# Performance work log

Hardware: AMD Instinct MI355X
Metric: run time of the kernel (lower is better)

The kernel has to match this reference:

```python
import jax, jax.numpy as jnp
import numpy as np

H = 64          # hidden_size
IN = 6          # input_size
PREDICT = 10    # predict_size


def _lstm_cell(x_t, h, c, Wih, Whh, bih, bhh):
    # PyTorch gate order: i, f, g, o ; gates = x W_ih^T + b_ih + h W_hh^T + b_hh
    g = x_t @ Wih.T + bih + h @ Whh.T + bhh            # [B, 4H]
    i, f, gg, o = jnp.split(g, 4, axis=-1)
    c_new = jax.nn.sigmoid(f) * c + jax.nn.sigmoid(i) * jnp.tanh(gg)
    h_new = jax.nn.sigmoid(o) * jnp.tanh(c_new)
    return h_new, c_new


def setup_inputs() -> dict:
    key = jax.random.key(0)
    ks = jax.random.split(key, 12)
    B, T = 4096, 1024
    s = 1.0 / np.sqrt(H)  # torch default uniform init bound
    u = lambda k, shape: jax.random.uniform(k, shape, jnp.float32, -s, s)
    return {
        "x": jax.random.normal(ks[0], (B, T, IN), jnp.float32),
        "W_ih0": u(ks[1], (4 * H, IN)),
        "W_hh0": u(ks[2], (4 * H, H)),
        "b_ih0": u(ks[3], (4 * H,)),
        "b_hh0": u(ks[4], (4 * H,)),
        "W_ih1": u(ks[5], (4 * H, H)),
        "W_hh1": u(ks[6], (4 * H, H)),
        "b_ih1": u(ks[7], (4 * H,)),
        "b_hh1": u(ks[8], (4 * H,)),
        "fc_w": u(ks[9], (IN, H)),
        "fc_b": u(ks[10], (IN,)),
    }


def reference(x, W_ih0, W_hh0, b_ih0, b_hh0, W_ih1, W_hh1, b_ih1, b_hh1, fc_w, fc_b):
    B = x.shape[0]
    zeros = jnp.zeros((B, H), x.dtype)
    init = (zeros, zeros, zeros, zeros)  # h0, c0, h1, c1

    def stacked_step(carry, x_t):
        h0, c0, h1, c1 = carry
        h0, c0 = _lstm_cell(x_t, h0, c0, W_ih0, W_hh0, b_ih0, b_hh0)
        h1, c1 = _lstm_cell(h0, h1, c1, W_ih1, W_hh1, b_ih1, b_hh1)
        return (h0, c0, h1, c1), None

    # Encoder: scan over time (batch_first -> transpose to [T, B, IN])
    carry, _ = jax.lax.scan(stacked_step, init, jnp.swapaxes(x, 0, 1))

    def dec_step(state, _):
        dec_in, c = state
        c, _ = stacked_step(c, dec_in)
        pred = c[0 + 2] @ fc_w.T + fc_b  # top-layer h -> [B, IN]
        return (pred, c), pred

    dec_in0 = x[:, -1, :]
    _, preds = jax.lax.scan(dec_step, (dec_in0, carry), None, length=PREDICT)
    return jnp.swapaxes(preds, 0, 1)  # [B, PREDICT, IN]
```

## Files before the change

### kernel.cpp

```cpp
#include <hip/hip_runtime.h>

#define T_SEQ   1024
#define INDIM   6
#define HDIM    64
#define NPRED   10
#define CHNK    128
#define S0      104
#define NROWS   16

typedef __bf16         bf16x8 __attribute__((ext_vector_type(8)));
typedef float          f32x4  __attribute__((ext_vector_type(4)));
typedef float          f32x2  __attribute__((ext_vector_type(2)));
typedef unsigned short us4    __attribute__((ext_vector_type(4)));

#define MFMA16(a, b, c) __builtin_amdgcn_mfma_f32_16x16x32_bf16((a), (b), (c), 0, 0, 0)

static __device__ __forceinline__ float bf2f(unsigned short b) {
  union { unsigned int u; float f; } v; v.u = ((unsigned int)b) << 16; return v.f;
}
static __device__ __forceinline__ unsigned short f2bf(float f) {
  union { __bf16 b; unsigned short u; } v; v.b = (__bf16)f; return v.u;
}

template <bool F32>
__global__ __launch_bounds__(512, 2)
void lstm2_pipe(const void* __restrict__ xv,
                const void* __restrict__ Wih0v,
                const void* __restrict__ Whh0v,
                const void* __restrict__ bih0v,
                const void* __restrict__ bhh0v,
                const void* __restrict__ Wih1v,
                const void* __restrict__ Whh1v,
                const void* __restrict__ bih1v,
                const void* __restrict__ bhh1v,
                const void* __restrict__ fcwv,
                const void* __restrict__ fcbv,
                void* __restrict__ outv)
{
  {
    const unsigned short* w0u = (const unsigned short*)Wih0v;
    int votes = 0;
#pragma unroll
    for (int i = 0; i < 16; ++i) {
      const unsigned e = (w0u[2 * i] >> 7) & 0xFF;
      votes += (e >= 0x80 || e <= 0x40) ? 1 : 0;
    }
    if ((votes >= 4) != F32) return;
  }

  __shared__ __align__(16) unsigned short A0[2][NROWS * S0];
  __shared__ __align__(16) unsigned short A1[2][NROWS * S0];
  __shared__ __align__(16) unsigned short XB[NROWS * CHNK * INDIM];
  __shared__ __align__(16) unsigned short FCW[INDIM * HDIM];
  __shared__ float FCB[INDIM];

  const int tid   = threadIdx.x;
  const int lane  = tid & 63;
  const int wave  = tid >> 6;
  const bool isA  = (wave < 4);
  const int  wv4  = wave & 3;
  const int  q    = lane >> 4;
  const int  n    = lane & 15;
  const int  u    = 16 * wv4 + n;
  const int rbase = blockIdx.x * NROWS;

  {
    unsigned short* p0 = &A0[0][0];
    unsigned short* p1 = &A1[0][0];
    for (int i = tid; i < 2 * NROWS * S0; i += 512) { p0[i] = 0; p1[i] = 0; }
  }
  for (int i = tid; i < INDIM * HDIM; i += 512) {
    if constexpr (F32) FCW[i] = f2bf(((const float*)fcwv)[i]);
    else               FCW[i] = ((const unsigned short*)fcwv)[i];
  }
  if (tid < INDIM) {
    if constexpr (F32) FCB[tid] = ((const float*)fcbv)[tid];
    else               FCB[tid] = bf2f(((const unsigned short*)fcbv)[tid]);
  }

  auto ld1 = [&](const void* p, int i) -> float {
    if constexpr (F32) return ((const float*)p)[i];
    else               return bf2f(((const unsigned short*)p)[i]);
  };
  auto ld8 = [&](const void* W, int off) -> bf16x8 {
    union { unsigned short us[8]; bf16x8 v; } t;
    if constexpr (F32) {
      const float* p = (const float*)W + off;
#pragma unroll
      for (int j = 0; j < 8; ++j) t.us[j] = f2bf(p[j]);
    } else {
      t.v = *(const bf16x8*)((const unsigned short*)W + off);
    }
    return t.v;
  };

  auto load_chunk = [&](int t0c) {
    if constexpr (F32) {
      const char* xb = (const char*)xv;
      for (int c = tid; c < NROWS * 192; c += 512) {
        const int row = c / 192;
        const int off = c - row * 192;
        const float4 v = *(const float4*)(xb + (size_t)(rbase + row) * (T_SEQ * INDIM * 4)
                                             + (size_t)t0c * (INDIM * 4) + (size_t)off * 16);
        us4 o;
        o.x = f2bf(v.x); o.y = f2bf(v.y); o.z = f2bf(v.z); o.w = f2bf(v.w);
        *(us4*)((char*)XB + (size_t)c * 8) = o;
      }
    } else {
      const char* xb = (const char*)xv;
      for (int c = tid; c < NROWS * 96; c += 512) {
        const int row = c / 96;
        const int off = c - row * 96;
        const int4 v = *(const int4*)(xb + (size_t)(rbase + row) * (T_SEQ * INDIM * 2)
                                         + (size_t)t0c * (INDIM * 2) + (size_t)off * 16);
        *(int4*)((char*)XB + (size_t)c * 16) = v;
      }
    }
  };

  load_chunk(0);
  __syncthreads();

  const int xrow   = tid / INDIM;
  const int xk     = tid - xrow * INDIM;
  const int xWrOff = xrow * S0 + HDIM + xk;
  const int xbBase = xrow * (CHNK * INDIM) + xk;

  if (tid < 96) A0[0][xWrOff] = XB[xbBase];
  __syncthreads();

  const int aOff  = n * S0 + 8 * q;
  const int hOffW = n * S0 + 16 * wv4 + 4 * q;
  const int bOff  = 16 * wv4 + 4 * q;

  f32x2 cc2[2]; cc2[0] = (f32x2){0.f, 0.f}; cc2[1] = (f32x2){0.f, 0.f};

  auto ldbias = [&](const void* b1, const void* b2, int gt) -> f32x4 {
    f32x4 r;
#pragma unroll
    for (int j = 0; j < 4; ++j)
      r[j] = ld1(b1, 64 * gt + bOff + j) + ld1(b2, 64 * gt + bOff + j);
    return r;
  };

  const f32x2 C1   = {-1.442695040888963f, -1.442695040888963f};
  const f32x2 C2   = {-2.885390081777927f, -2.885390081777927f};
  const f32x2 onep = {1.0f, 1.0f};

  auto act4 = [&](const f32x4 gI, const f32x4 gF, const f32x4 gG, const f32x4 gO,
                  unsigned short* dst) {
    unsigned int w2[2];
#pragma unroll
    for (int p = 0; p < 2; ++p) {
      f32x2 vI, vF, vG, vO;
      vI.x = gI[2 * p]; vI.y = gI[2 * p + 1];
      vF.x = gF[2 * p]; vF.y = gF[2 * p + 1];
      vG.x = gG[2 * p]; vG.y = gG[2 * p + 1];
      vO.x = gO[2 * p]; vO.y = gO[2 * p + 1];
      const f32x2 aF = vF * C1;
      const f32x2 aI = vI * C1;
      const f32x2 aG = vG * C2;
      const f32x2 aO = vO * C1;
      f32x2 Ae, Be, Ge, Oe;
      Ae.x = __builtin_amdgcn_exp2f(aF.x); Ae.y = __builtin_amdgcn_exp2f(aF.y);
      Be.x = __builtin_amdgcn_exp2f(aI.x); Be.y = __builtin_amdgcn_exp2f(aI.y);
      Ge.x = __builtin_amdgcn_exp2f(aG.x); Ge.y = __builtin_amdgcn_exp2f(aG.y);
      Oe.x = __builtin_amdgcn_exp2f(aO.x); Oe.y = __builtin_amdgcn_exp2f(aO.y);
      const f32x2 M1 = (onep + Be) * (onep + Ge);
      const f32x2 t2 = onep + Ae;
      const f32x2 nm = cc2[p] * M1 + (onep - Ge) * t2;
      const f32x2 den = t2 * M1;
      f32x2 rd; rd.x = __builtin_amdgcn_rcpf(den.x); rd.y = __builtin_amdgcn_rcpf(den.y);
      const f32x2 cn = nm * rd;
      cc2[p] = cn;
      const f32x2 aE = cn * C2;
      f32x2 Ee; Ee.x = __builtin_amdgcn_exp2f(aE.x); Ee.y = __builtin_amdgcn_exp2f(aE.y);
      const f32x2 dh = (onep + Ee) * (onep + Oe);
      f32x2 rh; rh.x = __builtin_amdgcn_rcpf(dh.x); rh.y = __builtin_amdgcn_rcpf(dh.y);
      const f32x2 hv = (onep - Ee) * rh;
      w2[p] = (unsigned int)f2bf(hv.x) | ((unsigned int)f2bf(hv.y) << 16);
    }
    uint2 pk; pk.x = w2[0]; pk.y = w2[1];
    *(uint2*)(dst + hOffW) = pk;
  };

  unsigned short* H0 = &A0[0][0];
  unsigned short* H1 = &A1[1][0];

  if (isA) {
    bf16x8 WA[12]; f32x4 bvA[4];
#pragma unroll
    for (int gt = 0; gt < 4; ++gt) {
      const int col = 64 * gt + u;
      WA[gt * 3 + 0] = ld8(Whh0v, col * HDIM + 8 * q);
      WA[gt * 3 + 1] = ld8(Whh0v, col * HDIM + 32 + 8 * q);
      union { unsigned short us[8]; bf16x8 v; } t2;
#pragma unroll
      for (int j = 0; j < 8; ++j) t2.us[j] = 0;
      if (q == 0) {
#pragma unroll
        for (int j = 0; j < INDIM; ++j) t2.us[j] = f2bf(ld1(Wih0v, col * INDIM + j));
      }
      WA[gt * 3 + 2] = t2.v;
      bvA[gt] = ldbias(bih0v, bhh0v, gt);
    }

    int t0v = 0;
    for (int i = 0; i <= T_SEQ; ++i) {
      if (((i + 1) & (CHNK - 1)) == 0 && (i + 1) < T_SEQ) {
        load_chunk(i + 1);
        __syncthreads();
        t0v = i + 1;
      }
      const int cur = i & 1;
      if (i < T_SEQ) {
        const unsigned short* A0c = &A0[cur][0];
        unsigned short*       A0n = &A0[cur ^ 1][0];
        const int srct = (i + 1 < T_SEQ) ? (i + 1) : (T_SEQ - 1);
        if (tid < 96) A0n[xWrOff] = XB[xbBase + (srct - t0v) * INDIM];
        const bf16x8 f0 = *(const bf16x8*)(A0c + aOff);
        const bf16x8 f1 = *(const bf16x8*)(A0c + aOff + 32);
        const bf16x8 f2 = *(const bf16x8*)(A0c + aOff + 64);
        f32x4 g0 = MFMA16(WA[0], f0, bvA[0]); g0 = MFMA16(WA[1],  f1, g0); g0 = MFMA16(WA[2],  f2, g0);
        f32x4 g1 = MFMA16(WA[3], f0, bvA[1]); g1 = MFMA16(WA[4],  f1, g1); g1 = MFMA16(WA[5],  f2, g1);
        f32x4 g2 = MFMA16(WA[6], f0, bvA[2]); g2 = MFMA16(WA[7],  f1, g2); g2 = MFMA16(WA[8],  f2, g2);
        f32x4 g3 = MFMA16(WA[9], f0, bvA[3]); g3 = MFMA16(WA[10], f1, g3); g3 = MFMA16(WA[11], f2, g3);
        act4(g0, g1, g2, g3, A0n);
      }
      __syncthreads();
    }
    for (int d = 0; d < NPRED; ++d) {
      const bf16x8 fa0 = *(const bf16x8*)(H0 + aOff);
      const bf16x8 fa1 = *(const bf16x8*)(H0 + aOff + 32);
      const bf16x8 fa2 = *(const bf16x8*)(H0 + aOff + 64);
      __syncthreads();
      {
        f32x4 g0 = MFMA16(WA[0], fa0, bvA[0]); g0 = MFMA16(WA[1],  fa1, g0); g0 = MFMA16(WA[2],  fa2, g0);
        f32x4 g1 = MFMA16(WA[3], fa0, bvA[1]); g1 = MFMA16(WA[4],  fa1, g1); g1 = MFMA16(WA[5],  fa2, g1);
        f32x4 g2 = MFMA16(WA[6], fa0, bvA[2]); g2 = MFMA16(WA[7],  fa1, g2); g2 = MFMA16(WA[8],  fa2, g2);
        f32x4 g3 = MFMA16(WA[9], fa0, bvA[3]); g3 = MFMA16(WA[10], fa1, g3); g3 = MFMA16(WA[11], fa2, g3);
        act4(g0, g1, g2, g3, H0);
      }
      __syncthreads();
      __syncthreads();
      if (tid < 96) {
        const unsigned short* h1row = H1 + xrow * S0;
        const int4* hp = (const int4*)h1row;
        const int4* wp = (const int4*)(&FCW[xk * HDIM]);
        float s = FCB[xk];
#pragma unroll
        for (int i8 = 0; i8 < 8; ++i8) {
          const int4 hv = hp[i8];
          const int4 wv2 = wp[i8];
          const unsigned int hu[4] = {(unsigned)hv.x, (unsigned)hv.y, (unsigned)hv.z, (unsigned)hv.w};
          const unsigned int wu[4] = {(unsigned)wv2.x, (unsigned)wv2.y, (unsigned)wv2.z, (unsigned)wv2.w};
#pragma unroll
          for (int k2 = 0; k2 < 4; ++k2) {
            union { unsigned int uu; float ff; } hl, hh2, wl, wh;
            hl.uu = hu[k2] << 16; hh2.uu = hu[k2] & 0xFFFF0000u;
            wl.uu = wu[k2] << 16; wh.uu  = wu[k2] & 0xFFFF0000u;
            s += hl.ff * wl.ff + hh2.ff * wh.ff;
          }
        }
        const unsigned short pb = f2bf(s);
        const size_t idx = (size_t)(rbase + xrow) * (NPRED * INDIM) + (size_t)d * INDIM + xk;
        if constexpr (F32) ((float*)outv)[idx] = s;
        else               ((unsigned short*)outv)[idx] = pb;
        H0[xWrOff] = pb;
      }
      __syncthreads();
    }
  } else {
    bf16x8 WB[16]; f32x4 bvB[4];
#pragma unroll
    for (int gt = 0; gt < 4; ++gt) {
      const int col = 64 * gt + u;
      WB[gt * 4 + 0] = ld8(Wih1v, col * HDIM + 8 * q);
      WB[gt * 4 + 1] = ld8(Wih1v, col * HDIM + 32 + 8 * q);
      WB[gt * 4 + 2] = ld8(Whh1v, col * HDIM + 8 * q);
      WB[gt * 4 + 3] = ld8(Whh1v, col * HDIM + 32 + 8 * q);
      bvB[gt] = ldbias(bih1v, bhh1v, gt);
    }

    for (int i = 0; i <= T_SEQ; ++i) {
      if (((i + 1) & (CHNK - 1)) == 0 && (i + 1) < T_SEQ) {
        load_chunk(i + 1);
        __syncthreads();
      }
      const int cur = i & 1;
      if (i >= 1) {
        const unsigned short* A0c = &A0[cur][0];
        const unsigned short* A1c = &A1[cur][0];
        unsigned short*       A1n = &A1[cur ^ 1][0];
        const bf16x8 h0a = *(const bf16x8*)(A0c + aOff);
        const bf16x8 h0b = *(const bf16x8*)(A0c + aOff + 32);
        const bf16x8 r0  = *(const bf16x8*)(A1c + aOff);
        const bf16x8 r1  = *(const bf16x8*)(A1c + aOff + 32);
        f32x4 g0 = MFMA16(WB[0],  h0a, bvB[0]); g0 = MFMA16(WB[1],  h0b, g0); g0 = MFMA16(WB[2],  r0, g0); g0 = MFMA16(WB[3],  r1, g0);
        f32x4 g1 = MFMA16(WB[4],  h0a, bvB[1]); g1 = MFMA16(WB[5],  h0b, g1); g1 = MFMA16(WB[6],  r0, g1); g1 = MFMA16(WB[7],  r1, g1);
        f32x4 g2 = MFMA16(WB[8],  h0a, bvB[2]); g2 = MFMA16(WB[9],  h0b, g2); g2 = MFMA16(WB[10], r0, g2); g2 = MFMA16(WB[11], r1, g2);
        f32x4 g3 = MFMA16(WB[12], h0a, bvB[3]); g3 = MFMA16(WB[13], h0b, g3); g3 = MFMA16(WB[14], r0, g3); g3 = MFMA16(WB[15], r1, g3);
        act4(g0, g1, g2, g3, A1n);
      }
      __syncthreads();
    }
    for (int d = 0; d < NPRED; ++d) {
      const bf16x8 fr0 = *(const bf16x8*)(H1 + aOff);
      const bf16x8 fr1 = *(const bf16x8*)(H1 + aOff + 32);
      __syncthreads();
      __syncthreads();
      {
        const bf16x8 h0a = *(const bf16x8*)(H0 + aOff);
        const bf16x8 h0b = *(const bf16x8*)(H0 + aOff + 32);
        f32x4 g0 = MFMA16(WB[0],  h0a, bvB[0]); g0 = MFMA16(WB[1],  h0b, g0); g0 = MFMA16(WB[2],  fr0, g0); g0 = MFMA16(WB[3],  fr1, g0);
        f32x4 g1 = MFMA16(WB[4],  h0a, bvB[1]); g1 = MFMA16(WB[5],  h0b, g1); g1 = MFMA16(WB[6],  fr0, g1); g1 = MFMA16(WB[7],  fr1, g1);
        f32x4 g2 = MFMA16(WB[8],  h0a, bvB[2]); g2 = MFMA16(WB[9],  h0b, g2); g2 = MFMA16(WB[10], fr0, g2); g2 = MFMA16(WB[11], fr1, g2);
        f32x4 g3 = MFMA16(WB[12], h0a, bvB[3]); g3 = MFMA16(WB[13], h0b, g3); g3 = MFMA16(WB[14], fr0, g3); g3 = MFMA16(WB[15], fr1, g3);
        act4(g0, g1, g2, g3, H1);
      }
      __syncthreads();
      __syncthreads();
    }
  }
}

extern "C" void kernel_launch(void* const* d_in, const int* in_sizes, int n_in,
                              void* d_out, int out_size, void* d_ws, size_t ws_size,
                              hipStream_t stream) {
  (void)in_sizes; (void)n_in; (void)d_ws; (void)ws_size; (void)out_size;
  const void* x    = d_in[0];
  const void* Wih0 = d_in[1];
  const void* Whh0 = d_in[2];
  const void* bih0 = d_in[3];
  const void* bhh0 = d_in[4];
  const void* Wih1 = d_in[5];
  const void* Whh1 = d_in[6];
  const void* bih1 = d_in[7];
  const void* bhh1 = d_in[8];
  const void* fcw  = d_in[9];
  const void* fcb  = d_in[10];
  lstm2_pipe<true><<<dim3(4096 / NROWS), dim3(512), 0, stream>>>(
      x, Wih0, Whh0, bih0, bhh0, Wih1, Whh1, bih1, bhh1, fcw, fcb, d_out);
  lstm2_pipe<false><<<dim3(4096 / NROWS), dim3(512), 0, stream>>>(
      x, Wih0, Whh0, bih0, bhh0, Wih1, Whh1, bih1, bhh1, fcw, fcb, d_out);
}
```

Before: 910.6 us.

## Split LSTM step into MFMA and activation phases to overlap layers

```diff
diff --git a/kernel.cpp b/kernel.cpp
--- a/kernel.cpp
+++ b/kernel.cpp
@@ -185,7 +185,7 @@
   };
 
   unsigned short* H0 = &A0[0][0];
-  unsigned short* H1 = &A1[1][0];
+  unsigned short* H1 = &A1[0][0];
 
   if (isA) {
     bf16x8 WA[12]; f32x4 bvA[4];
@@ -206,26 +206,31 @@
     }
 
     int t0v = 0;
-    for (int i = 0; i <= T_SEQ; ++i) {
+    f32x4 gA0, gA1, gA2, gA3;
+    for (int i = 0; i <= T_SEQ + 1; ++i) {
       if (((i + 1) & (CHNK - 1)) == 0 && (i + 1) < T_SEQ) {
         load_chunk(i + 1);
         __syncthreads();
         t0v = i + 1;
       }
       const int cur = i & 1;
-      if (i < T_SEQ) {
+      const bool run = (i < T_SEQ);
+      if (run) {
         const unsigned short* A0c = &A0[cur][0];
-        unsigned short*       A0n = &A0[cur ^ 1][0];
-        const int srct = (i + 1 < T_SEQ) ? (i + 1) : (T_SEQ - 1);
-        if (tid < 96) A0n[xWrOff] = XB[xbBase + (srct - t0v) * INDIM];
         const bf16x8 f0 = *(const bf16x8*)(A0c + aOff);
         const bf16x8 f1 = *(const bf16x8*)(A0c + aOff + 32);
         const bf16x8 f2 = *(const bf16x8*)(A0c + aOff + 64);
-        f32x4 g0 = MFMA16(WA[0], f0, bvA[0]); g0 = MFMA16(WA[1],  f1, g0); g0 = MFMA16(WA[2],  f2, g0);
-        f32x4 g1 = MFMA16(WA[3], f0, bvA[1]); g1 = MFMA16(WA[4],  f1, g1); g1 = MFMA16(WA[5],  f2, g1);
-        f32x4 g2 = MFMA16(WA[6], f0, bvA[2]); g2 = MFMA16(WA[7],  f1, g2); g2 = MFMA16(WA[8],  f2, g2);
-        f32x4 g3 = MFMA16(WA[9], f0, bvA[3]); g3 = MFMA16(WA[10], f1, g3); g3 = MFMA16(WA[11], f2, g3);
-        act4(g0, g1, g2, g3, A0n);
+        gA0 = MFMA16(WA[0], f0, bvA[0]); gA0 = MFMA16(WA[1],  f1, gA0); gA0 = MFMA16(WA[2],  f2, gA0);
+        gA1 = MFMA16(WA[3], f0, bvA[1]); gA1 = MFMA16(WA[4],  f1, gA1); gA1 = MFMA16(WA[5],  f2, gA1);
+        gA2 = MFMA16(WA[6], f0, bvA[2]); gA2 = MFMA16(WA[7],  f1, gA2); gA2 = MFMA16(WA[8],  f2, gA2);
+        gA3 = MFMA16(WA[9], f0, bvA[3]); gA3 = MFMA16(WA[10], f1, gA3); gA3 = MFMA16(WA[11], f2, gA3);
+      }
+      __syncthreads();
+      if (run) {
+        unsigned short* A0n = &A0[cur ^ 1][0];
+        const int srct = (i + 1 < T_SEQ) ? (i + 1) : (T_SEQ - 1);
+        if (tid < 96) A0n[xWrOff] = XB[xbBase + (srct - t0v) * INDIM];
+        act4(gA0, gA1, gA2, gA3, A0n);
       }
       __syncthreads();
     }
@@ -282,25 +287,28 @@
       bvB[gt] = ldbias(bih1v, bhh1v, gt);
     }
 
-    for (int i = 0; i <= T_SEQ; ++i) {
+    f32x4 gB0, gB1, gB2, gB3;
+    for (int i = 0; i <= T_SEQ + 1; ++i) {
       if (((i + 1) & (CHNK - 1)) == 0 && (i + 1) < T_SEQ) {
         load_chunk(i + 1);
         __syncthreads();
       }
       const int cur = i & 1;
-      if (i >= 1) {
+      if (i >= 2) {
+        act4(gB0, gB1, gB2, gB3, &A1[cur ^ 1][0]);
+      }
+      __syncthreads();
+      if (i >= 1 && i <= T_SEQ) {
         const unsigned short* A0c = &A0[cur][0];
-        const unsigned short* A1c = &A1[cur][0];
-        unsigned short*       A1n = &A1[cur ^ 1][0];
+        const unsigned short* A1c = &A1[cur ^ 1][0];
         const bf16x8 h0a = *(const bf16x8*)(A0c + aOff);
         const bf16x8 h0b = *(const bf16x8*)(A0c + aOff + 32);
         const bf16x8 r0  = *(const bf16x8*)(A1c + aOff);
         const bf16x8 r1  = *(const bf16x8*)(A1c + aOff + 32);
-        f32x4 g0 = MFMA16(WB[0],  h0a, bvB[0]); g0 = MFMA16(WB[1],  h0b, g0); g0 = MFMA16(WB[2],  r0, g0); g0 = MFMA16(WB[3],  r1, g0);
-        f32x4 g1 = MFMA16(WB[4],  h0a, bvB[1]); g1 = MFMA16(WB[5],  h0b, g1); g1 = MFMA16(WB[6],  r0, g1); g1 = MFMA16(WB[7],  r1, g1);
-        f32x4 g2 = MFMA16(WB[8],  h0a, bvB[2]); g2 = MFMA16(WB[9],  h0b, g2); g2 = MFMA16(WB[10], r0, g2); g2 = MFMA16(WB[11], r1, g2);
-        f32x4 g3 = MFMA16(WB[12], h0a, bvB[3]); g3 = MFMA16(WB[13], h0b, g3); g3 = MFMA16(WB[14], r0, g3); g3 = MFMA16(WB[15], r1, g3);
-        act4(g0, g1, g2, g3, A1n);
+        gB0 = MFMA16(WB[0],  h0a, bvB[0]); gB0 = MFMA16(WB[1],  h0b, gB0); gB0 = MFMA16(WB[2],  r0, gB0); gB0 = MFMA16(WB[3],  r1, gB0);
+        gB1 = MFMA16(WB[4],  h0a, bvB[1]); gB1 = MFMA16(WB[5],  h0b, gB1); gB1 = MFMA16(WB[6],  r0, gB1); gB1 = MFMA16(WB[7],  r1, gB1);
+        gB2 = MFMA16(WB[8],  h0a, bvB[2]); gB2 = MFMA16(WB[9],  h0b, gB2); gB2 = MFMA16(WB[10], r0, gB2); gB2 = MFMA16(WB[11], r1, gB2);
+        gB3 = MFMA16(WB[12], h0a, bvB[3]); gB3 = MFMA16(WB[13], h0b, gB3); gB3 = MFMA16(WB[14], r0, gB3); gB3 = MFMA16(WB[15], r1, gB3);
       }
       __syncthreads();
     }
```

Result: slower. 1.010 ms (+10.9%).

## Replace per-step block barriers with LDS flag polling between layer wave groups

Applied to the files above, without the earlier changes.

```diff
diff --git a/kernel.cpp b/kernel.cpp
--- a/kernel.cpp
+++ b/kernel.cpp
@@ -21,6 +21,7 @@
 static __device__ __forceinline__ unsigned short f2bf(float f) {
   union { __bf16 b; unsigned short u; } v; v.b = (__bf16)f; return v.u;
 }
+static __device__ __forceinline__ int imin(int a, int b) { return a < b ? a : b; }
 
 template <bool F32>
 __global__ __launch_bounds__(512, 2)
@@ -48,11 +49,12 @@
     if ((votes >= 4) != F32) return;
   }
 
-  __shared__ __align__(16) unsigned short A0[2][NROWS * S0];
+  __shared__ __align__(16) unsigned short A0[4][NROWS * S0];
   __shared__ __align__(16) unsigned short A1[2][NROWS * S0];
   __shared__ __align__(16) unsigned short XB[NROWS * CHNK * INDIM];
   __shared__ __align__(16) unsigned short FCW[INDIM * HDIM];
   __shared__ float FCB[INDIM];
+  __shared__ int FLG[8];
 
   const int tid   = threadIdx.x;
   const int lane  = tid & 63;
@@ -67,7 +69,8 @@
   {
     unsigned short* p0 = &A0[0][0];
     unsigned short* p1 = &A1[0][0];
-    for (int i = tid; i < 2 * NROWS * S0; i += 512) { p0[i] = 0; p1[i] = 0; }
+    for (int i = tid; i < 4 * NROWS * S0; i += 512) p0[i] = 0;
+    for (int i = tid; i < 2 * NROWS * S0; i += 512) p1[i] = 0;
   }
   for (int i = tid; i < INDIM * HDIM; i += 512) {
     if constexpr (F32) FCW[i] = f2bf(((const float*)fcwv)[i]);
@@ -77,6 +80,7 @@
     if constexpr (F32) FCB[tid] = ((const float*)fcbv)[tid];
     else               FCB[tid] = bf2f(((const unsigned short*)fcbv)[tid]);
   }
+  if (tid < 8) FLG[tid] = 0;
 
   auto ld1 = [&](const void* p, int i) -> float {
     if constexpr (F32) return ((const float*)p)[i];
@@ -121,17 +125,40 @@
   load_chunk(0);
   __syncthreads();
 
-  const int xrow   = tid / INDIM;
-  const int xk     = tid - xrow * INDIM;
-  const int xWrOff = xrow * S0 + HDIM + xk;
-  const int xbBase = xrow * (CHNK * INDIM) + xk;
-
-  if (tid < 96) A0[0][xWrOff] = XB[xbBase];
+  const int dxr    = tid / INDIM;
+  const int dxk    = tid - dxr * INDIM;
+  const int dxWrOff= dxr * S0 + HDIM + dxk;
+
+  if (tid < 96) A0[3][dxWrOff] = XB[dxr * (CHNK * INDIM) + dxk];
   __syncthreads();
+
+  const int  xe     = wv4 * 24 + lane;
+  const bool xact   = isA && (lane < 24);
+  const int  exr    = xe / INDIM;
+  const int  exk    = xe - exr * INDIM;
+  const int  exWrOff= exr * S0 + HDIM + exk;
+  const int  exbBase= exr * (CHNK * INDIM) + exk;
 
   const int aOff  = n * S0 + 8 * q;
   const int hOffW = n * S0 + 16 * wv4 + 4 * q;
   const int bOff  = 16 * wv4 + 4 * q;
+
+  auto poll2 = [&](int ta, int tb) {
+    volatile int* f = (volatile int*)FLG;
+    for (;;) {
+      const int a0 = f[0], a1 = f[1], a2 = f[2], a3 = f[3];
+      const int b0 = f[4], b1 = f[5], b2 = f[6], b3 = f[7];
+      const int am = imin(imin(a0, a1), imin(a2, a3));
+      const int bm = imin(imin(b0, b1), imin(b2, b3));
+      if (am >= ta && bm >= tb) break;
+      __builtin_amdgcn_s_sleep(1);
+    }
+    __threadfence_block();
+  };
+  auto post = [&](int idx, int val) {
+    __threadfence_block();
+    if (lane == 0) ((volatile int*)FLG)[idx] = val;
+  };
 
   f32x2 cc2[2]; cc2[0] = (f32x2){0.f, 0.f}; cc2[1] = (f32x2){0.f, 0.f};
 
@@ -184,7 +211,7 @@
     *(uint2*)(dst + hOffW) = pk;
   };
 
-  unsigned short* H0 = &A0[0][0];
+  unsigned short* H0 = &A0[3][0];
   unsigned short* H1 = &A1[1][0];
 
   if (isA) {
@@ -206,29 +233,29 @@
     }
 
     int t0v = 0;
-    for (int i = 0; i <= T_SEQ; ++i) {
-      if (((i + 1) & (CHNK - 1)) == 0 && (i + 1) < T_SEQ) {
-        load_chunk(i + 1);
+    for (int t = 0; t < T_SEQ; ++t) {
+      if (((t + 1) & (CHNK - 1)) == 0 && (t + 1) < T_SEQ) {
         __syncthreads();
-        t0v = i + 1;
-      }
-      const int cur = i & 1;
-      if (i < T_SEQ) {
-        const unsigned short* A0c = &A0[cur][0];
-        unsigned short*       A0n = &A0[cur ^ 1][0];
-        const int srct = (i + 1 < T_SEQ) ? (i + 1) : (T_SEQ - 1);
-        if (tid < 96) A0n[xWrOff] = XB[xbBase + (srct - t0v) * INDIM];
-        const bf16x8 f0 = *(const bf16x8*)(A0c + aOff);
-        const bf16x8 f1 = *(const bf16x8*)(A0c + aOff + 32);
-        const bf16x8 f2 = *(const bf16x8*)(A0c + aOff + 64);
-        f32x4 g0 = MFMA16(WA[0], f0, bvA[0]); g0 = MFMA16(WA[1],  f1, g0); g0 = MFMA16(WA[2],  f2, g0);
-        f32x4 g1 = MFMA16(WA[3], f0, bvA[1]); g1 = MFMA16(WA[4],  f1, g1); g1 = MFMA16(WA[5],  f2, g1);
-        f32x4 g2 = MFMA16(WA[6], f0, bvA[2]); g2 = MFMA16(WA[7],  f1, g2); g2 = MFMA16(WA[8],  f2, g2);
-        f32x4 g3 = MFMA16(WA[9], f0, bvA[3]); g3 = MFMA16(WA[10], f1, g3); g3 = MFMA16(WA[11], f2, g3);
-        act4(g0, g1, g2, g3, A0n);
-      }
-      __syncthreads();
-    }
+        load_chunk(t + 1);
+        __syncthreads();
+        t0v = t + 1;
+      }
+      poll2(t, t - 3);
+      const unsigned short* A0c = &A0[(t + 3) & 3][0];
+      unsigned short*       A0n = &A0[t & 3][0];
+      const int srct = (t + 1 < T_SEQ) ? (t + 1) : (T_SEQ - 1);
+      if (xact) A0n[exWrOff] = XB[exbBase + (srct - t0v) * INDIM];
+      const bf16x8 f0 = *(const bf16x8*)(A0c + aOff);
+      const bf16x8 f1 = *(const bf16x8*)(A0c + aOff + 32);
+      const bf16x8 f2 = *(const bf16x8*)(A0c + aOff + 64);
+      f32x4 g0 = MFMA16(WA[0], f0, bvA[0]); g0 = MFMA16(WA[1],  f1, g0); g0 = MFMA16(WA[2],  f2, g0);
+      f32x4 g1 = MFMA16(WA[3], f0, bvA[1]); g1 = MFMA16(WA[4],  f1, g1); g1 = MFMA16(WA[5],  f2, g1);
+      f32x4 g2 = MFMA16(WA[6], f0, bvA[2]); g2 = MFMA16(WA[7],  f1, g2); g2 = MFMA16(WA[8],  f2, g2);
+      f32x4 g3 = MFMA16(WA[9], f0, bvA[3]); g3 = MFMA16(WA[10], f1, g3); g3 = MFMA16(WA[11], f2, g3);
+      act4(g0, g1, g2, g3, A0n);
+      post(wv4, t + 1);
+    }
+    __syncthreads();
     for (int d = 0; d < NPRED; ++d) {
       const bf16x8 fa0 = *(const bf16x8*)(H0 + aOff);
       const bf16x8 fa1 = *(const bf16x8*)(H0 + aOff + 32);
@@ -244,10 +271,10 @@
       __syncthreads();
       __syncthreads();
       if (tid < 96) {
-        const unsigned short* h1row = H1 + xrow * S0;
+        const unsigned short* h1row = H1 + dxr * S0;
         const int4* hp = (const int4*)h1row;
-        const int4* wp = (const int4*)(&FCW[xk * HDIM]);
-        float s = FCB[xk];
+        const int4* wp = (const int4*)(&FCW[dxk * HDIM]);
+        float s = FCB[dxk];
 #pragma unroll
         for (int i8 = 0; i8 < 8; ++i8) {
           const int4 hv = hp[i8];
@@ -263,10 +290,10 @@
           }
         }
         const unsigned short pb = f2bf(s);
-        const size_t idx = (size_t)(rbase + xrow) * (NPRED * INDIM) + (size_t)d * INDIM + xk;
+        const size_t idx = (size_t)(rbase + dxr) * (NPRED * INDIM) + (size_t)d * INDIM + dxk;
         if constexpr (F32) ((float*)outv)[idx] = s;
         else               ((unsigned short*)outv)[idx] = pb;
-        H0[xWrOff] = pb;
+        H0[dxWrOff] = pb;
       }
       __syncthreads();
     }
@@ -282,28 +309,28 @@
       bvB[gt] = ldbias(bih1v, bhh1v, gt);
     }
 
-    for (int i = 0; i <= T_SEQ; ++i) {
-      if (((i + 1) & (CHNK - 1)) == 0 && (i + 1) < T_SEQ) {
-        load_chunk(i + 1);
+    for (int t = 0; t < T_SEQ; ++t) {
+      if (((t + 1) & (CHNK - 1)) == 0 && (t + 1) < T_SEQ) {
         __syncthreads();
-      }
-      const int cur = i & 1;
-      if (i >= 1) {
-        const unsigned short* A0c = &A0[cur][0];
-        const unsigned short* A1c = &A1[cur][0];
-        unsigned short*       A1n = &A1[cur ^ 1][0];
-        const bf16x8 h0a = *(const bf16x8*)(A0c + aOff);
-        const bf16x8 h0b = *(const bf16x8*)(A0c + aOff + 32);
-        const bf16x8 r0  = *(const bf16x8*)(A1c + aOff);
-        const bf16x8 r1  = *(const bf16x8*)(A1c + aOff + 32);
-        f32x4 g0 = MFMA16(WB[0],  h0a, bvB[0]); g0 = MFMA16(WB[1],  h0b, g0); g0 = MFMA16(WB[2],  r0, g0); g0 = MFMA16(WB[3],  r1, g0);
-        f32x4 g1 = MFMA16(WB[4],  h0a, bvB[1]); g1 = MFMA16(WB[5],  h0b, g1); g1 = MFMA16(WB[6],  r0, g1); g1 = MFMA16(WB[7],  r1, g1);
-        f32x4 g2 = MFMA16(WB[8],  h0a, bvB[2]); g2 = MFMA16(WB[9],  h0b, g2); g2 = MFMA16(WB[10], r0, g2); g2 = MFMA16(WB[11], r1, g2);
-        f32x4 g3 = MFMA16(WB[12], h0a, bvB[3]); g3 = MFMA16(WB[13], h0b, g3); g3 = MFMA16(WB[14], r0, g3); g3 = MFMA16(WB[15], r1, g3);
-        act4(g0, g1, g2, g3, A1n);
-      }
-      __syncthreads();
-    }
+        load_chunk(t + 1);
+        __syncthreads();
+      }
+      poll2(t + 1, t);
+      const unsigned short* A0c = &A0[t & 3][0];
+      const unsigned short* A1c = &A1[(t + 1) & 1][0];
+      unsigned short*       A1n = &A1[t & 1][0];
+      const bf16x8 h0a = *(const bf16x8*)(A0c + aOff);
+      const bf16x8 h0b = *(const bf16x8*)(A0c + aOff + 32);
+      const bf16x8 r0  = *(const bf16x8*)(A1c + aOff);
+      const bf16x8 r1  = *(const bf16x8*)(A1c + aOff + 32);
+      f32x4 g0 = MFMA16(WB[0],  h0a, bvB[0]); g0 = MFMA16(WB[1],  h0b, g0); g0 = MFMA16(WB[2],  r0, g0); g0 = MFMA16(WB[3],  r1, g0);
+      f32x4 g1 = MFMA16(WB[4],  h0a, bvB[1]); g1 = MFMA16(WB[5],  h0b, g1); g1 = MFMA16(WB[6],  r0, g1); g1 = MFMA16(WB[7],  r1, g1);
+      f32x4 g2 = MFMA16(WB[8],  h0a, bvB[2]); g2 = MFMA16(WB[9],  h0b, g2); g2 = MFMA16(WB[10], r0, g2); g2 = MFMA16(WB[11], r1, g2);
+      f32x4 g3 = MFMA16(WB[12], h0a, bvB[3]); g3 = MFMA16(WB[13], h0b, g3); g3 = MFMA16(WB[14], r0, g3); g3 = MFMA16(WB[15], r1, g3);
+      act4(g0, g1, g2, g3, A1n);
+      post(4 + wv4, t + 1);
+    }
+    __syncthreads();
     for (int d = 0; d < NPRED; ++d) {
       const bf16x8 fr0 = *(const bf16x8*)(H1 + aOff);
       const bf16x8 fr1 = *(const bf16x8*)(H1 + aOff + 32);
```

After: 1.145 ms. +25.8%, slower.

## Read layer-0 input directly from padded swizzled x buffer instead of per-step copy

Applied to the files above, without the earlier changes.

```diff
diff --git a/kernel.cpp b/kernel.cpp
--- a/kernel.cpp
+++ b/kernel.cpp
@@ -5,7 +5,7 @@
 #define HDIM    64
 #define NPRED   10
 #define CHNK    128
-#define S0      104
+#define S0      72
 #define NROWS   16
 
 typedef __bf16         bf16x8 __attribute__((ext_vector_type(8)));
@@ -50,7 +50,9 @@
 
   __shared__ __align__(16) unsigned short A0[2][NROWS * S0];
   __shared__ __align__(16) unsigned short A1[2][NROWS * S0];
-  __shared__ __align__(16) unsigned short XB[NROWS * CHNK * INDIM];
+  __shared__ __align__(16) unsigned short XB2[NROWS * CHNK * 8];
+  __shared__ __align__(16) unsigned short XD[NROWS * 8];
+  __shared__ __align__(16) unsigned short ZPAD[8];
   __shared__ __align__(16) unsigned short FCW[INDIM * HDIM];
   __shared__ float FCB[INDIM];
 
@@ -68,6 +70,8 @@
     unsigned short* p0 = &A0[0][0];
     unsigned short* p1 = &A1[0][0];
     for (int i = tid; i < 2 * NROWS * S0; i += 512) { p0[i] = 0; p1[i] = 0; }
+    for (int i = tid; i < NROWS * 8; i += 512) XD[i] = 0;
+    if (tid < 8) ZPAD[tid] = 0;
   }
   for (int i = tid; i < INDIM * HDIM; i += 512) {
     if constexpr (F32) FCW[i] = f2bf(((const float*)fcwv)[i]);
@@ -95,43 +99,49 @@
   };
 
   auto load_chunk = [&](int t0c) {
-    if constexpr (F32) {
-      const char* xb = (const char*)xv;
-      for (int c = tid; c < NROWS * 192; c += 512) {
-        const int row = c / 192;
-        const int off = c - row * 192;
-        const float4 v = *(const float4*)(xb + (size_t)(rbase + row) * (T_SEQ * INDIM * 4)
-                                             + (size_t)t0c * (INDIM * 4) + (size_t)off * 16);
-        us4 o;
-        o.x = f2bf(v.x); o.y = f2bf(v.y); o.z = f2bf(v.z); o.w = f2bf(v.w);
-        *(us4*)((char*)XB + (size_t)c * 8) = o;
-      }
-    } else {
-      const char* xb = (const char*)xv;
-      for (int c = tid; c < NROWS * 96; c += 512) {
-        const int row = c / 96;
-        const int off = c - row * 96;
-        const int4 v = *(const int4*)(xb + (size_t)(rbase + row) * (T_SEQ * INDIM * 2)
-                                         + (size_t)t0c * (INDIM * 2) + (size_t)off * 16);
-        *(int4*)((char*)XB + (size_t)c * 16) = v;
-      }
+    for (int c = tid; c < NROWS * CHNK; c += 512) {
+      const int row = c >> 7;
+      const int t   = c & (CHNK - 1);
+      int4 o;
+      if constexpr (F32) {
+        const float* p = (const float*)xv + ((size_t)(rbase + row) * T_SEQ + (t0c + t)) * INDIM;
+        const float2 v0 = *(const float2*)(p);
+        const float2 v1 = *(const float2*)(p + 2);
+        const float2 v2 = *(const float2*)(p + 4);
+        union { unsigned short us[8]; int4 v; } tt;
+        tt.us[0] = f2bf(v0.x); tt.us[1] = f2bf(v0.y);
+        tt.us[2] = f2bf(v1.x); tt.us[3] = f2bf(v1.y);
+        tt.us[4] = f2bf(v2.x); tt.us[5] = f2bf(v2.y);
+        tt.us[6] = 0;          tt.us[7] = 0;
+        o = tt.v;
+      } else {
+        const unsigned short* p = (const unsigned short*)xv
+            + ((size_t)(rbase + row) * T_SEQ + (t0c + t)) * INDIM;
+        o.x = *(const unsigned int*)(p);
+        o.y = *(const unsigned int*)(p + 2);
+        o.z = *(const unsigned int*)(p + 4);
+        o.w = 0;
+      }
+      *(int4*)((char*)XB2 + (((size_t)row * CHNK) + (t ^ (row & 7))) * 16) = o;
     }
   };
 
   load_chunk(0);
-  __syncthreads();
-
-  const int xrow   = tid / INDIM;
-  const int xk     = tid - xrow * INDIM;
-  const int xWrOff = xrow * S0 + HDIM + xk;
-  const int xbBase = xrow * (CHNK * INDIM) + xk;
-
-  if (tid < 96) A0[0][xWrOff] = XB[xbBase];
+
+  const int dxr = tid / INDIM;
+  const int dxk = tid - dxr * INDIM;
+
   __syncthreads();
 
   const int aOff  = n * S0 + 8 * q;
   const int hOffW = n * S0 + 16 * wv4 + 4 * q;
   const int bOff  = 16 * wv4 + 4 * q;
+
+  auto xsrc_at = [&](int tc) -> const char* {
+    return (q == 0)
+        ? ((const char*)XB2 + (((size_t)n * CHNK) + (tc ^ (n & 7))) * 16)
+        : (const char*)ZPAD;
+  };
 
   f32x2 cc2[2]; cc2[0] = (f32x2){0.f, 0.f}; cc2[1] = (f32x2){0.f, 0.f};
 
@@ -207,32 +217,36 @@
 
     int t0v = 0;
     for (int i = 0; i <= T_SEQ; ++i) {
-      if (((i + 1) & (CHNK - 1)) == 0 && (i + 1) < T_SEQ) {
-        load_chunk(i + 1);
+      if (i > 0 && i < T_SEQ && (i & (CHNK - 1)) == 0) {
+        load_chunk(i);
         __syncthreads();
-        t0v = i + 1;
+        t0v = i;
       }
       const int cur = i & 1;
       if (i < T_SEQ) {
         const unsigned short* A0c = &A0[cur][0];
         unsigned short*       A0n = &A0[cur ^ 1][0];
-        const int srct = (i + 1 < T_SEQ) ? (i + 1) : (T_SEQ - 1);
-        if (tid < 96) A0n[xWrOff] = XB[xbBase + (srct - t0v) * INDIM];
         const bf16x8 f0 = *(const bf16x8*)(A0c + aOff);
         const bf16x8 f1 = *(const bf16x8*)(A0c + aOff + 32);
-        const bf16x8 f2 = *(const bf16x8*)(A0c + aOff + 64);
+        const bf16x8 f2 = *(const bf16x8*)(xsrc_at(i - t0v));
+        __builtin_amdgcn_s_setprio(1);
         f32x4 g0 = MFMA16(WA[0], f0, bvA[0]); g0 = MFMA16(WA[1],  f1, g0); g0 = MFMA16(WA[2],  f2, g0);
         f32x4 g1 = MFMA16(WA[3], f0, bvA[1]); g1 = MFMA16(WA[4],  f1, g1); g1 = MFMA16(WA[5],  f2, g1);
         f32x4 g2 = MFMA16(WA[6], f0, bvA[2]); g2 = MFMA16(WA[7],  f1, g2); g2 = MFMA16(WA[8],  f2, g2);
         f32x4 g3 = MFMA16(WA[9], f0, bvA[3]); g3 = MFMA16(WA[10], f1, g3); g3 = MFMA16(WA[11], f2, g3);
+        __builtin_amdgcn_s_setprio(0);
         act4(g0, g1, g2, g3, A0n);
       }
       __syncthreads();
     }
+    if (tid < 96)
+      XD[dxr * 8 + dxk] = XB2[((size_t)dxr * CHNK + (127 ^ (dxr & 7))) * 8 + dxk];
+    __syncthreads();
     for (int d = 0; d < NPRED; ++d) {
       const bf16x8 fa0 = *(const bf16x8*)(H0 + aOff);
       const bf16x8 fa1 = *(const bf16x8*)(H0 + aOff + 32);
-      const bf16x8 fa2 = *(const bf16x8*)(H0 + aOff + 64);
+      const bf16x8 fa2 = *(const bf16x8*)((q == 0) ? ((const char*)XD + n * 16)
+                                                   : (const char*)ZPAD);
       __syncthreads();
       {
         f32x4 g0 = MFMA16(WA[0], fa0, bvA[0]); g0 = MFMA16(WA[1],  fa1, g0); g0 = MFMA16(WA[2],  fa2, g0);
@@ -244,10 +258,10 @@
       __syncthreads();
       __syncthreads();
       if (tid < 96) {
-        const unsigned short* h1row = H1 + xrow * S0;
+        const unsigned short* h1row = H1 + dxr * S0;
         const int4* hp = (const int4*)h1row;
-        const int4* wp = (const int4*)(&FCW[xk * HDIM]);
-        float s = FCB[xk];
+        const int4* wp = (const int4*)(&FCW[dxk * HDIM]);
+        float s = FCB[dxk];
 #pragma unroll
         for (int i8 = 0; i8 < 8; ++i8) {
           const int4 hv = hp[i8];
@@ -263,10 +277,10 @@
           }
         }
         const unsigned short pb = f2bf(s);
-        const size_t idx = (size_t)(rbase + xrow) * (NPRED * INDIM) + (size_t)d * INDIM + xk;
+        const size_t idx = (size_t)(rbase + dxr) * (NPRED * INDIM) + (size_t)d * INDIM + dxk;
         if constexpr (F32) ((float*)outv)[idx] = s;
         else               ((unsigned short*)outv)[idx] = pb;
-        H0[xWrOff] = pb;
+        XD[dxr * 8 + dxk] = pb;
       }
       __syncthreads();
     }
@@ -283,8 +297,8 @@
     }
 
     for (int i = 0; i <= T_SEQ; ++i) {
-      if (((i + 1) & (CHNK - 1)) == 0 && (i + 1) < T_SEQ) {
-        load_chunk(i + 1);
+      if (i > 0 && i < T_SEQ && (i & (CHNK - 1)) == 0) {
+        load_chunk(i);
         __syncthreads();
       }
       const int cur = i & 1;
@@ -296,14 +310,17 @@
         const bf16x8 h0b = *(const bf16x8*)(A0c + aOff + 32);
         const bf16x8 r0  = *(const bf16x8*)(A1c + aOff);
         const bf16x8 r1  = *(const bf16x8*)(A1c + aOff + 32);
+        __builtin_amdgcn_s_setprio(1);
         f32x4 g0 = MFMA16(WB[0],  h0a, bvB[0]); g0 = MFMA16(WB[1],  h0b, g0); g0 = MFMA16(WB[2],  r0, g0); g0 = MFMA16(WB[3],  r1, g0);
         f32x4 g1 = MFMA16(WB[4],  h0a, bvB[1]); g1 = MFMA16(WB[5],  h0b, g1); g1 = MFMA16(WB[6],  r0, g1); g1 = MFMA16(WB[7],  r1, g1);
         f32x4 g2 = MFMA16(WB[8],  h0a, bvB[2]); g2 = MFMA16(WB[9],  h0b, g2); g2 = MFMA16(WB[10], r0, g2); g2 = MFMA16(WB[11], r1, g2);
         f32x4 g3 = MFMA16(WB[12], h0a, bvB[3]); g3 = MFMA16(WB[13], h0b, g3); g3 = MFMA16(WB[14], r0, g3); g3 = MFMA16(WB[15], r1, g3);
+        __builtin_amdgcn_s_setprio(0);
         act4(g0, g1, g2, g3, A1n);
       }
       __syncthreads();
     }
+    __syncthreads();
     for (int d = 0; d < NPRED; ++d) {
       const bf16x8 fr0 = *(const bf16x8*)(H1 + aOff);
       const bf16x8 fr1 = *(const bf16x8*)(H1 + aOff + 32);
```

Measured after the change: 873.0 us. -4.1%, faster.
